# Performance work log

Hardware: AMD Instinct MI355X
Metric: run time of the kernel (lower is better)

The kernel has to match this reference:

```python
import jax, jax.numpy as jnp
import numpy as np
from jax import lax

K = 16  # knn_k


def _mlp(x, W1, b1, W2, b2):
    h = jax.nn.gelu(x @ W1 + b1, approximate=False)  # torch nn.GELU default = exact
    return h @ W2 + b2


def setup_inputs() -> dict:
    key = jax.random.key(0)
    ks = jax.random.split(key, 10)
    B, N, F, H = 8, 4096, 64, 128

    def xav(k, shape):
        fan_in = shape[0]
        return (jax.random.normal(k, shape, jnp.float32) / np.sqrt(fan_in)).astype(jnp.float32)

    return {
        "coords": jax.random.normal(ks[0], (B, N, 3), jnp.float32),
        "features": jax.random.normal(ks[1], (B, N, F), jnp.float32),
        "inv_W1": xav(ks[2], (6, H)), "inv_b1": jnp.zeros((H,), jnp.float32),
        "inv_W2": xav(ks[3], (H, H)), "inv_b2": jnp.zeros((H,), jnp.float32),
        "feat_W1": xav(ks[4], (F, H)), "feat_b1": jnp.zeros((H,), jnp.float32),
        "feat_W2": xav(ks[5], (H, H)), "feat_b2": jnp.zeros((H,), jnp.float32),
        "sh_W1": xav(ks[6], (2 * H, H)), "sh_b1": jnp.zeros((H,), jnp.float32),
        "sh_W2": xav(ks[7], (H, H)), "sh_b2": jnp.zeros((H,), jnp.float32),
        "g0_W": xav(ks[8], (H, 1)), "g0_b": jnp.zeros((1,), jnp.float32),
    }


def _local_geometry(coords):
    # coords: [B,N,3]
    B, N, _ = coords.shape
    k = min(K, N - 1)
    # squared pairwise distances (monotone in euclidean dist -> same kNN indices)
    sq = jnp.sum(coords * coords, axis=-1)                    # [B,N]
    dist2 = sq[:, :, None] + sq[:, None, :] - 2.0 * jnp.einsum("bnd,bmd->bnm", coords, coords)
    dist2 = lax.stop_gradient(dist2)
    eye = jnp.eye(N, dtype=bool)
    dist2 = jnp.where(eye[None], jnp.inf, dist2)
    _, idx = lax.top_k(-dist2, k)                             # smallest-k -> [B,N,k]
    neighbors = jax.vmap(lambda c, i: c[i])(coords, idx)      # [B,N,k,3]
    relative = neighbors - coords[:, :, None, :]              # [B,N,k,3]
    cov = jnp.einsum("bnki,bnkj->bnij", relative, relative) / float(k)  # [B,N,3,3]
    evals, evecs = jnp.linalg.eigh(cov)                       # ascending
    normals = evecs[..., 0]                                   # smallest-eigval eigenvector, [B,N,3]
    center = coords.mean(axis=1, keepdims=True)
    outward = coords - center
    orient = jnp.sign(jnp.sum(normals * outward, axis=-1, keepdims=True))
    orient = jnp.where(orient == 0, 1.0, orient)
    normals = normals * orient
    normals = normals / jnp.maximum(jnp.linalg.norm(normals, axis=-1, keepdims=True), 1e-6)
    radius = jnp.linalg.norm(relative, axis=-1).mean(axis=-1, keepdims=True)   # [B,N,1]
    centered_radius = jnp.linalg.norm(outward, axis=-1, keepdims=True)
    eig_sum = jnp.maximum(evals.sum(axis=-1, keepdims=True), 1e-6)
    dominance = evals[..., 2:3] / eig_sum
    invariants = jnp.concatenate([evals, radius, centered_radius, dominance], axis=-1)  # [B,N,6]
    return normals, invariants


def reference(coords, features, inv_W1, inv_b1, inv_W2, inv_b2,
              feat_W1, feat_b1, feat_W2, feat_b2,
              sh_W1, sh_b1, sh_W2, sh_b2, g0_W, g0_b):
    normals, invariants = _local_geometry(coords)
    inv_h = _mlp(invariants, inv_W1, inv_b1, inv_W2, inv_b2)
    feat_h = _mlp(features, feat_W1, feat_b1, feat_W2, feat_b2)
    hidden = _mlp(jnp.concatenate([inv_h, feat_h], axis=-1), sh_W1, sh_b1, sh_W2, sh_b2)
    scalar = hidden @ g0_W + g0_b                                   # grade 0, [B,N,1]
    plane = jnp.stack([normals[..., 0], normals[..., 1], -normals[..., 2],
                       -jnp.sum(coords * normals, axis=-1)], axis=-1)  # grade 1, [B,N,4]
    biv = jnp.concatenate([normals, jnp.zeros_like(normals)], axis=-1)  # grade 2, [B,N,6]
    point = jnp.concatenate([coords, jnp.ones(coords.shape[:-1] + (1,), coords.dtype)], axis=-1)  # grade 3 OPNS point
    zero4 = jnp.zeros(coords.shape[:-1] + (1,), coords.dtype)            # grade 4
    return jnp.concatenate([scalar, plane, biv, point, zero4], axis=-1)  # [B,N,16]
```

## Files before the change

### kernel.cpp

```cpp
#include <hip/hip_runtime.h>
#include <hip/hip_bf16.h>

#define BB 8
#define NN 4096
#define FF 64
#define HH 128
#define KNN 16

typedef __attribute__((ext_vector_type(8))) short bf16x8;
typedef __attribute__((ext_vector_type(4))) short bf16x4;
typedef __attribute__((ext_vector_type(4))) float f32x4;

#define OFF_iW2 0
#define OFF_fW1 16384
#define OFF_fW2 24576
#define OFF_sW1 40960
#define OFF_sW2 73728
#define HI_SZ   90112

__device__ __forceinline__ float sq3(float x, float y, float z) {
    return fmaf(z, z, fmaf(y, y, __fmul_rn(x, x)));
}
__device__ __forceinline__ float dist2f(float px, float py, float pz, float psq, float4 cc) {
    float t = fmaf(pz, cc.z, fmaf(py, cc.y, __fmul_rn(px, cc.x)));
    return __fsub_rn(__fadd_rn(psq, cc.w), __fmul_rn(2.0f, t));
}

__device__ __forceinline__ short f2bf(float x) {
    unsigned u = __float_as_uint(x);
    u += 0x7fffu + ((u >> 16) & 1u);
    return (short)(u >> 16);
}
__device__ __forceinline__ float bf2f(short s) {
    return __uint_as_float(((unsigned)(unsigned short)s) << 16);
}

extern "C" __global__ __launch_bounds__(256)
void k_prep(const float* __restrict__ coords, float4* __restrict__ coords4, float* __restrict__ center,
            const float* __restrict__ iW2, const float* __restrict__ fW1,
            const float* __restrict__ fW2, const float* __restrict__ sW1,
            const float* __restrict__ sW2, short* __restrict__ wbf) {
    const int bx = blockIdx.x, tid = threadIdx.x;
    __shared__ float rx[256], ry[256], rz[256];
    if (bx < 8) {
        const int b = bx;
        float sx = 0.f, sy = 0.f, sz = 0.f;
        for (int n = tid; n < NN; n += 256) {
            const float* c = coords + (size_t)(b * NN + n) * 3;
            float x = c[0], y = c[1], z = c[2];
            coords4[b * NN + n] = make_float4(x, y, z, sq3(x, y, z));
            sx += x; sy += y; sz += z;
        }
        rx[tid] = sx; ry[tid] = sy; rz[tid] = sz;
        __syncthreads();
        for (int s = 128; s > 0; s >>= 1) {
            if (tid < s) { rx[tid] += rx[tid + s]; ry[tid] += ry[tid + s]; rz[tid] += rz[tid + s]; }
            __syncthreads();
        }
        if (tid == 0) {
            center[b * 4 + 0] = rx[0] * (1.0f / NN);
            center[b * 4 + 1] = ry[0] * (1.0f / NN);
            center[b * 4 + 2] = rz[0] * (1.0f / NN);
        }
    } else {
        const int wb = bx - 8;
        const int w = wb >> 4;
        const int xb = wb & 15;
        const float* W; int K; int off;
        if (w == 0)      { W = iW2; K = 128; off = OFF_iW2; }
        else if (w == 1) { W = fW1; K = 64;  off = OFF_fW1; }
        else if (w == 2) { W = fW2; K = 128; off = OFF_fW2; }
        else if (w == 3) { W = sW1; K = 256; off = OFF_sW1; }
        else             { W = sW2; K = 128; off = OFF_sW2; }
        short* hi = wbf + off;
        short* lo = wbf + HI_SZ + off;
        const int total = K * 128;
        for (int e = xb * 256 + tid; e < total; e += 4096) {
            int j = e & 7, lane = (e >> 3) & 63, ct = (e >> 9) & 7, kb = e >> 12;
            int k = kb * 32 + (lane >> 4) * 8 + j;
            int n = ct * 16 + (lane & 15);
            float v = W[k * 128 + n];
            short h = f2bf(v);
            float r = v - bf2f(h);
            hi[e] = h; lo[e] = f2bf(r);
        }
    }
}

#define JROT(app, aqq, apq, arp, arq, vp0, vp1, vp2, vq0, vq1, vq2) { \
    float tau_ = (aqq - app) / (2.0f * apq); \
    float tt_ = copysignf(1.0f, tau_) / (fabsf(tau_) + sqrtf(1.0f + tau_ * tau_)); \
    if (apq == 0.0f) tt_ = 0.0f; \
    float cc_ = 1.0f / sqrtf(1.0f + tt_ * tt_); \
    float ss_ = tt_ * cc_; \
    float app_n = cc_*cc_*app - 2.0f*cc_*ss_*apq + ss_*ss_*aqq; \
    float aqq_n = ss_*ss_*app + 2.0f*cc_*ss_*apq + cc_*cc_*aqq; \
    float apq_n = cc_*ss_*(app - aqq) + (cc_*cc_ - ss_*ss_)*apq; \
    float arp_n = cc_*arp - ss_*arq; \
    float arq_n = ss_*arp + cc_*arq; \
    app = app_n; aqq = aqq_n; apq = apq_n; arp = arp_n; arq = arq_n; \
    float t0_ = cc_*vp0 - ss_*vq0, t1_ = cc_*vp1 - ss_*vq1, t2_ = cc_*vp2 - ss_*vq2; \
    vq0 = ss_*vp0 + cc_*vq0; vq1 = ss_*vp1 + cc_*vq1; vq2 = ss_*vp2 + cc_*vq2; \
    vp0 = t0_; vp1 = t1_; vp2 = t2_; }

#define SWAPF(a, b) { float sw_ = a; a = b; b = sw_; }

__device__ __forceinline__ void ce(float& a, float& b) {
    float mn = fminf(a, b);
    b = fmaxf(a, b);
    a = mn;
}

__device__ __forceinline__ void sort16(float (&d)[16]) {
    ce(d[0],d[1]); ce(d[2],d[3]); ce(d[0],d[2]); ce(d[1],d[3]); ce(d[1],d[2]);
    ce(d[4],d[5]); ce(d[6],d[7]); ce(d[4],d[6]); ce(d[5],d[7]); ce(d[5],d[6]);
    ce(d[0],d[4]); ce(d[2],d[6]); ce(d[2],d[4]);
    ce(d[1],d[5]); ce(d[3],d[7]); ce(d[3],d[5]);
    ce(d[1],d[2]); ce(d[3],d[4]); ce(d[5],d[6]);
    ce(d[8],d[9]); ce(d[10],d[11]); ce(d[8],d[10]); ce(d[9],d[11]); ce(d[9],d[10]);
    ce(d[12],d[13]); ce(d[14],d[15]); ce(d[12],d[14]); ce(d[13],d[15]); ce(d[13],d[14]);
    ce(d[8],d[12]); ce(d[10],d[14]); ce(d[10],d[12]);
    ce(d[9],d[13]); ce(d[11],d[15]); ce(d[11],d[13]);
    ce(d[9],d[10]); ce(d[11],d[12]); ce(d[13],d[14]);
    ce(d[0],d[8]); ce(d[4],d[12]); ce(d[4],d[8]);
    ce(d[2],d[10]); ce(d[6],d[14]); ce(d[6],d[10]);
    ce(d[2],d[4]); ce(d[6],d[8]); ce(d[10],d[12]);
    ce(d[1],d[9]); ce(d[5],d[13]); ce(d[5],d[9]);
    ce(d[3],d[11]); ce(d[7],d[15]); ce(d[7],d[11]);
    ce(d[3],d[5]); ce(d[7],d[9]); ce(d[11],d[13]);
    ce(d[1],d[2]); ce(d[3],d[4]); ce(d[5],d[6]); ce(d[7],d[8]);
    ce(d[9],d[10]); ce(d[11],d[12]); ce(d[13],d[14]);
}

__device__ __forceinline__ void merge16(float (&dk)[16], float (&d)[16]) {
#pragma unroll
    for (int i = 0; i < 8; i++) {
        float a  = fminf(dk[i], d[15 - i]);
        float b2 = fminf(dk[15 - i], d[i]);
        d[i] = a; d[15 - i] = b2;
    }
#pragma unroll
    for (int j = 8; j > 0; j >>= 1)
#pragma unroll
        for (int i = 0; i < 16; i++) {
            int l = i ^ j;
            if (l > i) ce(d[i], d[l]);
        }
#pragma unroll
    for (int i = 0; i < 16; i++) dk[i] = d[i];
}

__device__ __forceinline__ void sort16i(int (&d)[16]) {
#pragma unroll
    for (int k = 2; k <= 16; k <<= 1) {
#pragma unroll
        for (int j = k >> 1; j > 0; j >>= 1) {
#pragma unroll
            for (int i = 0; i < 16; i++) {
                int l = i ^ j;
                if (l > i) {
                    int a = d[i], bq = d[l];
                    int mn = a < bq ? a : bq;
                    int mx = a < bq ? bq : a;
                    if ((i & k) == 0) { d[i] = mn; d[l] = mx; }
                    else              { d[i] = mx; d[l] = mn; }
                }
            }
        }
    }
}

extern "C" __global__ __launch_bounds__(512, 8)
void k_knn(const float4* __restrict__ coords4, const float* __restrict__ center,
           float* __restrict__ inv8g, float* __restrict__ out) {
    const int blk = blockIdx.x;
    const int b = blk >> 7;
    const int chunk = blk & 127;
    const int tid = threadIdx.x;
    const int h = tid & 15;
    const int pid = tid >> 4;
    const int n = chunk * 32 + pid;
    const float4* __restrict__ C = coords4 + b * NN;

    __shared__ __align__(16) float4 tile[1024];
    __shared__ unsigned short slist[512];
    __shared__ unsigned short tlist[256];
    __shared__ int cnt_s[32];
    __shared__ int cnt_t[32];

    if (tid < 32) { cnt_s[tid] = 0; cnt_t[tid] = 0; }

    float4 me = C[n];
    const float px = me.x, py = me.y, pz = me.z, psq = me.w;
    const float INF = __builtin_inff();

    float dk[KNN];
#pragma unroll
    for (int i = 0; i < KNN; i++) dk[i] = INF;

    for (int r = 0; r < 4; r++) {
        __syncthreads();
        tile[tid] = C[r * 1024 + tid];
        tile[tid + 512] = C[r * 1024 + tid + 512];
        __syncthreads();
#pragma unroll
        for (int bt = 0; bt < 4; bt++) {
            float d[16];
#pragma unroll
            for (int i = 0; i < 16; i++) {
                float4 cc = tile[bt * 256 + i * 16 + h];
                float dd = dist2f(px, py, pz, psq, cc);
                int g = r * 1024 + bt * 256 + i * 16 + h;
                d[i] = (g == n) ? INF : dd;
            }
            sort16(d);
            merge16(dk, d);
        }
    }

#pragma unroll
    for (int m = 1; m <= 8; m <<= 1) {
        float o[16];
#pragma unroll
        for (int i = 0; i < KNN; i++) o[i] = __shfl_xor(dk[i], m);
        merge16(dk, o);
    }
    const float d15 = dk[15];

    for (int r = 0; r < 4; r++) {
        __syncthreads();
        tile[tid] = C[r * 1024 + tid];
        tile[tid + 512] = C[r * 1024 + tid + 512];
        __syncthreads();
#pragma unroll 4
        for (int j16 = 0; j16 < 64; j16++) {
            float4 cc = tile[j16 * 16 + h];
            float d = dist2f(px, py, pz, psq, cc);
            int g = r * 1024 + j16 * 16 + h;
            if (g != n && d <= d15) {
                if (d < d15) {
                    int pos = atomicAdd(&cnt_s[pid], 1);
                    if (pos < 16) slist[pid * 16 + pos] = (unsigned short)g;
                } else {
                    int pos = atomicAdd(&cnt_t[pid], 1);
                    if (pos < 8) tlist[pid * 8 + pos] = (unsigned short)g;
                }
            }
        }
    }
    __syncthreads();

    if (tid < 32) {
        const int np = chunk * 32 + tid;
        float4 pme = C[np];
        int ns = cnt_s[tid]; ns = ns > 15 ? 15 : ns;
        int ids[16];
#pragma unroll
        for (int j = 0; j < 16; j++) {
            int tj = j - ns; tj = tj < 0 ? 0 : (tj > 7 ? 7 : tj);
            int sid = (int)slist[tid * 16 + j];
            int tie = (int)tlist[tid * 8 + tj];
            ids[j] = (j < ns) ? sid : tie;
        }
        sort16i(ids);

        float cxx = 0.f, cxy = 0.f, cxz = 0.f, cyy = 0.f, cyz = 0.f, czz = 0.f, radsum = 0.f;
#pragma unroll
        for (int j = 0; j < KNN; j++) {
            float4 cc = C[ids[j]];
            float rx = __fsub_rn(cc.x, pme.x), ry = __fsub_rn(cc.y, pme.y), rz = __fsub_rn(cc.z, pme.z);
            cxx = __fadd_rn(cxx, __fmul_rn(rx, rx));
            cxy = __fadd_rn(cxy, __fmul_rn(rx, ry));
            cxz = __fadd_rn(cxz, __fmul_rn(rx, rz));
            cyy = __fadd_rn(cyy, __fmul_rn(ry, ry));
            cyz = __fadd_rn(cyz, __fmul_rn(ry, rz));
            czz = __fadd_rn(czz, __fmul_rn(rz, rz));
            float rr = __fadd_rn(__fadd_rn(__fmul_rn(rx, rx), __fmul_rn(ry, ry)), __fmul_rn(rz, rz));
            radsum = __fadd_rn(radsum, sqrtf(rr));
        }
        const float inv_k = 1.0f / KNN;
        float a00 = cxx * inv_k, a01 = cxy * inv_k, a02 = cxz * inv_k;
        float a11 = cyy * inv_k, a12 = cyz * inv_k, a22 = czz * inv_k;

        float V00 = 1.f, V01 = 0.f, V02 = 0.f;
        float V10 = 0.f, V11 = 1.f, V12 = 0.f;
        float V20 = 0.f, V21 = 0.f, V22 = 1.f;
        for (int sweep = 0; sweep < 6; sweep++) {
            JROT(a00, a11, a01, a02, a12, V00, V10, V20, V01, V11, V21);
            JROT(a00, a22, a02, a01, a12, V00, V10, V20, V02, V12, V22);
            JROT(a11, a22, a12, a01, a02, V01, V11, V21, V02, V12, V22);
        }
        float e0 = a00, e1 = a11, e2 = a22;
        float x0 = V00, y0 = V10, z0 = V20;
        float x1 = V01, y1 = V11, z1 = V21;
        float x2 = V02, y2 = V12, z2 = V22;
        if (e0 > e1) { SWAPF(e0, e1); SWAPF(x0, x1); SWAPF(y0, y1); SWAPF(z0, z1); }
        if (e1 > e2) { SWAPF(e1, e2); SWAPF(x1, x2); SWAPF(y1, y2); SWAPF(z1, z2); }
        if (e0 > e1) { SWAPF(e0, e1); SWAPF(x0, x1); SWAPF(y0, y1); SWAPF(z0, z1); }

        float cx = center[b * 4 + 0], cy = center[b * 4 + 1], cz = center[b * 4 + 2];
        float ox = __fsub_rn(pme.x, cx), oy = __fsub_rn(pme.y, cy), oz = __fsub_rn(pme.z, cz);
        float dt = __fadd_rn(__fadd_rn(__fmul_rn(x0, ox), __fmul_rn(y0, oy)), __fmul_rn(z0, oz));
        float sgn = (dt >= 0.0f) ? 1.0f : -1.0f;
        x0 *= sgn; y0 *= sgn; z0 *= sgn;
        float nrm = sqrtf(__fadd_rn(__fadd_rn(__fmul_rn(x0, x0), __fmul_rn(y0, y0)), __fmul_rn(z0, z0)));
        float den = fmaxf(nrm, 1e-6f);
        x0 = x0 / den; y0 = y0 / den; z0 = z0 / den;

        float radius = radsum * inv_k;
        float crad = sqrtf(__fadd_rn(__fadd_rn(__fmul_rn(ox, ox), __fmul_rn(oy, oy)), __fmul_rn(oz, oz)));
        float esum = fmaxf(__fadd_rn(__fadd_rn(e0, e1), e2), 1e-6f);
        float dom = e2 / esum;

        float* ip = inv8g + (size_t)(b * NN + np) * 8;
        ip[0] = e0; ip[1] = e1; ip[2] = e2; ip[3] = radius; ip[4] = crad; ip[5] = dom;
        ip[6] = 0.f; ip[7] = 0.f;

        float pd = __fadd_rn(__fadd_rn(__fmul_rn(pme.x, x0), __fmul_rn(pme.y, y0)), __fmul_rn(pme.z, z0));
        float4* o = (float4*)(out + (size_t)(b * NN + np) * 16);
        o[0] = make_float4(0.0f, x0, y0, -z0);
        o[1] = make_float4(-pd, x0, y0, z0);
        o[2] = make_float4(0.0f, 0.0f, 0.0f, pme.x);
        o[3] = make_float4(pme.y, pme.z, 1.0f, 0.0f);
    }
}

__device__ __forceinline__ float gelu_exact(float x) {
    return 0.5f * x * (1.0f + erff(x * 0.70710678118654752440f));
}

template <int KB, bool INIT>
__device__ __forceinline__ void gemm_mfma(const short* Ab, const short* __restrict__ whi,
                                          const short* __restrict__ wlo,
                                          const float* __restrict__ bias,
                                          int wid, int lane, f32x4 acc[2]) {
    const int m16 = lane & 15, quad = lane >> 4;
    if (INIT) {
        float b0 = bias[wid * 16 + m16];
        acc[0] = (f32x4){b0, b0, b0, b0};
        acc[1] = acc[0];
    }
#pragma unroll 1
    for (int kb = 0; kb < KB; kb++) {
        bf16x8 a0 = *(const bf16x8*)(Ab + m16 * 136 + kb * 32 + quad * 8);
        bf16x8 a1 = *(const bf16x8*)(Ab + (m16 + 16) * 136 + kb * 32 + quad * 8);
        const int off = ((kb * 8 + wid) * 64 + lane) * 8;
        bf16x8 bh = *(const bf16x8*)(whi + off);
        bf16x8 bl = *(const bf16x8*)(wlo + off);
        acc[0] = __builtin_amdgcn_mfma_f32_16x16x32_bf16(a0, bh, acc[0], 0, 0, 0);
        acc[0] = __builtin_amdgcn_mfma_f32_16x16x32_bf16(a0, bl, acc[0], 0, 0, 0);
        acc[1] = __builtin_amdgcn_mfma_f32_16x16x32_bf16(a1, bh, acc[1], 0, 0, 0);
        acc[1] = __builtin_amdgcn_mfma_f32_16x16x32_bf16(a1, bl, acc[1], 0, 0, 0);
    }
}

__device__ __forceinline__ void acc_to_bf(short* dst, f32x4 acc[2], int wid, int lane, bool dogelu) {
    const int m16 = lane & 15, quad = lane >> 4;
#pragma unroll
    for (int mt = 0; mt < 2; mt++)
#pragma unroll
        for (int i = 0; i < 4; i++) {
            float v = acc[mt][i];
            if (dogelu) v = gelu_exact(v);
            dst[(mt * 16 + quad * 4 + i) * 136 + wid * 16 + m16] = f2bf(v);
        }
}

extern "C" __global__ __launch_bounds__(512, 8)
void k_mlp(const float* __restrict__ features, const short* __restrict__ wbf,
           const float* __restrict__ iW1, const float* __restrict__ ib1,
           const float* __restrict__ ib2,
           const float* __restrict__ fb1, const float* __restrict__ fb2,
           const float* __restrict__ sb1, const float* __restrict__ sb2,
           const float* __restrict__ gW, const float* __restrict__ gb,
           const float* __restrict__ inv8g, float* __restrict__ out) {
    const int blk = blockIdx.x;
    const int b = blk >> 7;
    const int chunk = blk & 127;
    const int tid = threadIdx.x;

    __shared__ __align__(16) float inv8[256];
    __shared__ float sc[32];
    __shared__ __align__(16) short Abf[32 * 136];
    __shared__ __align__(16) short FHbf[32 * 136];

    const int wid = tid >> 6, lane = tid & 63;
    const short* w_iW2h = wbf + OFF_iW2; const short* w_iW2l = wbf + HI_SZ + OFF_iW2;
    const short* w_fW1h = wbf + OFF_fW1; const short* w_fW1l = wbf + HI_SZ + OFF_fW1;
    const short* w_fW2h = wbf + OFF_fW2; const short* w_fW2l = wbf + HI_SZ + OFF_fW2;
    const short* w_sW1h = wbf + OFF_sW1; const short* w_sW1l = wbf + HI_SZ + OFF_sW1;
    const short* w_sW2h = wbf + OFF_sW2; const short* w_sW2l = wbf + HI_SZ + OFF_sW2;
    f32x4 acc[2];

    if (tid < 256) inv8[tid] = inv8g[(size_t)(b * NN + chunk * 32) * 8 + tid];
    if (tid < 32) sc[tid] = gb[0];
    {
        int row = tid >> 4, c4 = (tid & 15) * 4;
        const float* s = features + (size_t)(b * NN + chunk * 32 + row) * FF + c4;
        float4 v = *(const float4*)s;
        bf16x4 pk;
        pk[0] = f2bf(v.x); pk[1] = f2bf(v.y); pk[2] = f2bf(v.z); pk[3] = f2bf(v.w);
        *(bf16x4*)(Abf + row * 136 + c4) = pk;
    }
    __syncthreads();

    gemm_mfma<2, true>(Abf, w_fW1h, w_fW1l, fb1, wid, lane, acc);
    __syncthreads();
    acc_to_bf(Abf, acc, wid, lane, true);
    __syncthreads();

    gemm_mfma<4, true>(Abf, w_fW2h, w_fW2l, fb2, wid, lane, acc);
    __syncthreads();
    acc_to_bf(FHbf, acc, wid, lane, false);

    {
        const int cg = tid & 31, pg = tid >> 5;
        const int c0 = cg * 4, p0 = pg * 2;
        float4 bb = *(const float4*)(ib1 + c0);
        float a2[2][4];
#pragma unroll
        for (int i = 0; i < 2; i++) { a2[i][0] = bb.x; a2[i][1] = bb.y; a2[i][2] = bb.z; a2[i][3] = bb.w; }
#pragma unroll
        for (int k = 0; k < 6; k++) {
            float4 w = *(const float4*)(iW1 + k * HH + c0);
#pragma unroll
            for (int i = 0; i < 2; i++) {
                float a = inv8[(p0 + i) * 8 + k];
                a2[i][0] = fmaf(a, w.x, a2[i][0]);
                a2[i][1] = fmaf(a, w.y, a2[i][1]);
                a2[i][2] = fmaf(a, w.z, a2[i][2]);
                a2[i][3] = fmaf(a, w.w, a2[i][3]);
            }
        }
#pragma unroll
        for (int i = 0; i < 2; i++) {
            bf16x4 pk;
            pk[0] = f2bf(gelu_exact(a2[i][0])); pk[1] = f2bf(gelu_exact(a2[i][1]));
            pk[2] = f2bf(gelu_exact(a2[i][2])); pk[3] = f2bf(gelu_exact(a2[i][3]));
            *(bf16x4*)(Abf + (p0 + i) * 136 + c0) = pk;
        }
    }
    __syncthreads();

    gemm_mfma<4, true>(Abf, w_iW2h, w_iW2l, ib2, wid, lane, acc);
    __syncthreads();
    acc_to_bf(Abf, acc, wid, lane, false);
    __syncthreads();

    gemm_mfma<4, true>(Abf, w_sW1h, w_sW1l, sb1, wid, lane, acc);
    gemm_mfma<4, false>(FHbf, w_sW1h + 16384, w_sW1l + 16384, nullptr, wid, lane, acc);
    __syncthreads();
    acc_to_bf(Abf, acc, wid, lane, true);
    __syncthreads();

    gemm_mfma<4, true>(Abf, w_sW2h, w_sW2l, sb2, wid, lane, acc);
    {
        const int m16 = lane & 15, quad = lane >> 4;
        float g = gW[wid * 16 + m16];
#pragma unroll
        for (int mt = 0; mt < 2; mt++)
#pragma unroll
            for (int i = 0; i < 4; i++)
                atomicAdd(&sc[mt * 16 + quad * 4 + i], acc[mt][i] * g);
    }
    __syncthreads();
    if (tid < 32) out[(size_t)(b * NN + chunk * 32 + tid) * 16] = sc[tid];
}

extern "C" void kernel_launch(void* const* d_in, const int* in_sizes, int n_in,
                              void* d_out, int out_size, void* d_ws, size_t ws_size,
                              hipStream_t stream) {
    const float* coords   = (const float*)d_in[0];
    const float* features = (const float*)d_in[1];
    const float* iW1 = (const float*)d_in[2],  * ib1 = (const float*)d_in[3];
    const float* iW2 = (const float*)d_in[4],  * ib2 = (const float*)d_in[5];
    const float* fW1 = (const float*)d_in[6],  * fb1 = (const float*)d_in[7];
    const float* fW2 = (const float*)d_in[8],  * fb2 = (const float*)d_in[9];
    const float* sW1 = (const float*)d_in[10], * sb1 = (const float*)d_in[11];
    const float* sW2 = (const float*)d_in[12], * sb2 = (const float*)d_in[13];
    const float* gW  = (const float*)d_in[14], * gb  = (const float*)d_in[15];
    float* out = (float*)d_out;

    char* ws = (char*)d_ws;
    float4* coords4 = (float4*)ws;
    float* center   = (float*)(ws + 524288);
    short* wbf      = (short*)(ws + 524416);
    float* inv8g    = (float*)(ws + 884864);

    hipLaunchKernelGGL(k_prep, dim3(88), dim3(256), 0, stream,
                       coords, coords4, center, iW2, fW1, fW2, sW1, sW2, wbf);
    hipLaunchKernelGGL(k_knn, dim3(1024), dim3(512), 0, stream, coords4, center, inv8g, out);
    hipLaunchKernelGGL(k_mlp, dim3(1024), dim3(512), 0, stream, features, wbf,
                       iW1, ib1, ib2, fb1, fb2, sb1, sb2, gW, gb, inv8g, out);
}
```

Measured before the change: 263.8 us.

## Double-buffer kNN tiles, hoist self-exclusion, and process 64 points per MLP block

The kNN kernel now double-buffers the coordinate tile in shared memory, so the next 1024-point tile loads while the current one is scanned, removing one barrier per round. The self-exclusion compare now runs only in the tile that holds the query point. merge16 now works in place instead of copying back. The MLP kernel handles two 32-point sub-tiles per block, reusing each loaded weight fragment for twice the MFMA work, and launches half as many blocks with a lower occupancy hint. This doubles LDS use and may raise register pressure.

```diff
diff --git a/kernel.cpp b/kernel.cpp
--- a/kernel.cpp
+++ b/kernel.cpp
@@ -132,22 +132,20 @@
     ce(d[9],d[10]); ce(d[11],d[12]); ce(d[13],d[14]);
 }
 
-__device__ __forceinline__ void merge16(float (&dk)[16], float (&d)[16]) {
+__device__ __forceinline__ void merge16(float (&dk)[16], const float (&d)[16]) {
 #pragma unroll
     for (int i = 0; i < 8; i++) {
         float a  = fminf(dk[i], d[15 - i]);
         float b2 = fminf(dk[15 - i], d[i]);
-        d[i] = a; d[15 - i] = b2;
+        dk[i] = a; dk[15 - i] = b2;
     }
 #pragma unroll
     for (int j = 8; j > 0; j >>= 1)
 #pragma unroll
         for (int i = 0; i < 16; i++) {
             int l = i ^ j;
-            if (l > i) ce(d[i], d[l]);
-        }
-#pragma unroll
-    for (int i = 0; i < 16; i++) dk[i] = d[i];
+            if (l > i) ce(dk[i], dk[l]);
+        }
 }
 
 __device__ __forceinline__ void sort16i(int (&d)[16]) {
@@ -168,6 +166,23 @@
             }
         }
     }
+}
+
+template <bool CHK>
+__device__ __forceinline__ void batch16(const float4* __restrict__ T, int bt, int h, int sl_local,
+                                        float px, float py, float pz, float psq,
+                                        float (&dk)[16]) {
+    const float INF = __builtin_inff();
+    float d[16];
+#pragma unroll
+    for (int i = 0; i < 16; i++) {
+        float4 cc = T[bt * 256 + i * 16 + h];
+        float dd = dist2f(px, py, pz, psq, cc);
+        if (CHK) d[i] = (bt * 256 + i * 16 + h) == sl_local ? INF : dd;
+        else     d[i] = dd;
+    }
+    sort16(d);
+    merge16(dk, d);
 }
 
 extern "C" __global__ __launch_bounds__(512, 8)
@@ -182,7 +197,7 @@
     const int n = chunk * 32 + pid;
     const float4* __restrict__ C = coords4 + b * NN;
 
-    __shared__ __align__(16) float4 tile[1024];
+    __shared__ __align__(16) float4 tile[2][1024];
     __shared__ unsigned short slist[512];
     __shared__ unsigned short tlist[256];
     __shared__ int cnt_s[32];
@@ -194,29 +209,40 @@
     const float px = me.x, py = me.y, pz = me.z, psq = me.w;
     const float INF = __builtin_inff();
 
+    const int r_self  = chunk >> 5;
+    const int bt_self = (chunk >> 3) & 3;
+    const int sl_local = n & 1023;
+
     float dk[KNN];
 #pragma unroll
     for (int i = 0; i < KNN; i++) dk[i] = INF;
 
+    tile[0][tid] = C[tid];
+    tile[0][tid + 512] = C[tid + 512];
     for (int r = 0; r < 4; r++) {
         __syncthreads();
-        tile[tid] = C[r * 1024 + tid];
-        tile[tid + 512] = C[r * 1024 + tid + 512];
-        __syncthreads();
-#pragma unroll
-        for (int bt = 0; bt < 4; bt++) {
-            float d[16];
-#pragma unroll
-            for (int i = 0; i < 16; i++) {
-                float4 cc = tile[bt * 256 + i * 16 + h];
-                float dd = dist2f(px, py, pz, psq, cc);
-                int g = r * 1024 + bt * 256 + i * 16 + h;
-                d[i] = (g == n) ? INF : dd;
-            }
-            sort16(d);
-            merge16(dk, d);
-        }
-    }
+        if (r < 3) {
+            tile[(r + 1) & 1][tid] = C[(r + 1) * 1024 + tid];
+            tile[(r + 1) & 1][tid + 512] = C[(r + 1) * 1024 + tid + 512];
+        }
+        const float4* T = tile[r & 1];
+        if (r != r_self) {
+            batch16<false>(T, 0, h, sl_local, px, py, pz, psq, dk);
+            batch16<false>(T, 1, h, sl_local, px, py, pz, psq, dk);
+            batch16<false>(T, 2, h, sl_local, px, py, pz, psq, dk);
+            batch16<false>(T, 3, h, sl_local, px, py, pz, psq, dk);
+        } else {
+#pragma unroll
+            for (int bt = 0; bt < 4; bt++) {
+                if (bt == bt_self) batch16<true>(T, bt, h, sl_local, px, py, pz, psq, dk);
+                else               batch16<false>(T, bt, h, sl_local, px, py, pz, psq, dk);
+            }
+        }
+    }
+
+    __syncthreads();
+    tile[0][tid] = C[tid];
+    tile[0][tid + 512] = C[tid + 512];
 
 #pragma unroll
     for (int m = 1; m <= 8; m <<= 1) {
@@ -229,21 +255,42 @@
 
     for (int r = 0; r < 4; r++) {
         __syncthreads();
-        tile[tid] = C[r * 1024 + tid];
-        tile[tid + 512] = C[r * 1024 + tid + 512];
-        __syncthreads();
+        if (r < 3) {
+            tile[(r + 1) & 1][tid] = C[(r + 1) * 1024 + tid];
+            tile[(r + 1) & 1][tid + 512] = C[(r + 1) * 1024 + tid + 512];
+        }
+        const float4* T = tile[r & 1];
+        if (r != r_self) {
 #pragma unroll 4
-        for (int j16 = 0; j16 < 64; j16++) {
-            float4 cc = tile[j16 * 16 + h];
-            float d = dist2f(px, py, pz, psq, cc);
-            int g = r * 1024 + j16 * 16 + h;
-            if (g != n && d <= d15) {
-                if (d < d15) {
-                    int pos = atomicAdd(&cnt_s[pid], 1);
-                    if (pos < 16) slist[pid * 16 + pos] = (unsigned short)g;
-                } else {
-                    int pos = atomicAdd(&cnt_t[pid], 1);
-                    if (pos < 8) tlist[pid * 8 + pos] = (unsigned short)g;
+            for (int j16 = 0; j16 < 64; j16++) {
+                float4 cc = T[j16 * 16 + h];
+                float d = dist2f(px, py, pz, psq, cc);
+                if (d <= d15) {
+                    int g = r * 1024 + j16 * 16 + h;
+                    if (d < d15) {
+                        int pos = atomicAdd(&cnt_s[pid], 1);
+                        if (pos < 16) slist[pid * 16 + pos] = (unsigned short)g;
+                    } else {
+                        int pos = atomicAdd(&cnt_t[pid], 1);
+                        if (pos < 8) tlist[pid * 8 + pos] = (unsigned short)g;
+                    }
+                }
+            }
+        } else {
+#pragma unroll 4
+            for (int j16 = 0; j16 < 64; j16++) {
+                float4 cc = T[j16 * 16 + h];
+                float d = dist2f(px, py, pz, psq, cc);
+                int cl = j16 * 16 + h;
+                if (cl != sl_local && d <= d15) {
+                    int g = r * 1024 + cl;
+                    if (d < d15) {
+                        int pos = atomicAdd(&cnt_s[pid], 1);
+                        if (pos < 16) slist[pid * 16 + pos] = (unsigned short)g;
+                    } else {
+                        int pos = atomicAdd(&cnt_t[pid], 1);
+                        if (pos < 8) tlist[pid * 8 + pos] = (unsigned short)g;
+                    }
                 }
             }
         }
@@ -330,27 +377,35 @@
 }
 
 template <int KB, bool INIT>
-__device__ __forceinline__ void gemm_mfma(const short* Ab, const short* __restrict__ whi,
-                                          const short* __restrict__ wlo,
-                                          const float* __restrict__ bias,
-                                          int wid, int lane, f32x4 acc[2]) {
+__device__ __forceinline__ void gemm_mfma2(const short* Ab0, const short* Ab1,
+                                           const short* __restrict__ whi,
+                                           const short* __restrict__ wlo,
+                                           const float* __restrict__ bias,
+                                           int wid, int lane, f32x4 acc0[2], f32x4 acc1[2]) {
     const int m16 = lane & 15, quad = lane >> 4;
     if (INIT) {
         float b0 = bias[wid * 16 + m16];
-        acc[0] = (f32x4){b0, b0, b0, b0};
-        acc[1] = acc[0];
+        acc0[0] = (f32x4){b0, b0, b0, b0};
+        acc0[1] = acc0[0]; acc1[0] = acc0[0]; acc1[1] = acc0[0];
     }
 #pragma unroll 1
     for (int kb = 0; kb < KB; kb++) {
-        bf16x8 a0 = *(const bf16x8*)(Ab + m16 * 136 + kb * 32 + quad * 8);
-        bf16x8 a1 = *(const bf16x8*)(Ab + (m16 + 16) * 136 + kb * 32 + quad * 8);
         const int off = ((kb * 8 + wid) * 64 + lane) * 8;
         bf16x8 bh = *(const bf16x8*)(whi + off);
         bf16x8 bl = *(const bf16x8*)(wlo + off);
-        acc[0] = __builtin_amdgcn_mfma_f32_16x16x32_bf16(a0, bh, acc[0], 0, 0, 0);
-        acc[0] = __builtin_amdgcn_mfma_f32_16x16x32_bf16(a0, bl, acc[0], 0, 0, 0);
-        acc[1] = __builtin_amdgcn_mfma_f32_16x16x32_bf16(a1, bh, acc[1], 0, 0, 0);
-        acc[1] = __builtin_amdgcn_mfma_f32_16x16x32_bf16(a1, bl, acc[1], 0, 0, 0);
+        const int ao = m16 * 136 + kb * 32 + quad * 8;
+        bf16x8 a00 = *(const bf16x8*)(Ab0 + ao);
+        bf16x8 a01 = *(const bf16x8*)(Ab0 + ao + 16 * 136);
+        bf16x8 a10 = *(const bf16x8*)(Ab1 + ao);
+        bf16x8 a11 = *(const bf16x8*)(Ab1 + ao + 16 * 136);
+        acc0[0] = __builtin_amdgcn_mfma_f32_16x16x32_bf16(a00, bh, acc0[0], 0, 0, 0);
+        acc0[0] = __builtin_amdgcn_mfma_f32_16x16x32_bf16(a00, bl, acc0[0], 0, 0, 0);
+        acc0[1] = __builtin_amdgcn_mfma_f32_16x16x32_bf16(a01, bh, acc0[1], 0, 0, 0);
+        acc0[1] = __builtin_amdgcn_mfma_f32_16x16x32_bf16(a01, bl, acc0[1], 0, 0, 0);
+        acc1[0] = __builtin_amdgcn_mfma_f32_16x16x32_bf16(a10, bh, acc1[0], 0, 0, 0);
+        acc1[0] = __builtin_amdgcn_mfma_f32_16x16x32_bf16(a10, bl, acc1[0], 0, 0, 0);
+        acc1[1] = __builtin_amdgcn_mfma_f32_16x16x32_bf16(a11, bh, acc1[1], 0, 0, 0);
+        acc1[1] = __builtin_amdgcn_mfma_f32_16x16x32_bf16(a11, bl, acc1[1], 0, 0, 0);
     }
 }
 
@@ -366,7 +421,7 @@
         }
 }
 
-extern "C" __global__ __launch_bounds__(512, 8)
+extern "C" __global__ __launch_bounds__(512, 4)
 void k_mlp(const float* __restrict__ features, const short* __restrict__ wbf,
            const float* __restrict__ iW1, const float* __restrict__ ib1,
            const float* __restrict__ ib2,
@@ -375,14 +430,15 @@
            const float* __restrict__ gW, const float* __restrict__ gb,
            const float* __restrict__ inv8g, float* __restrict__ out) {
     const int blk = blockIdx.x;
-    const int b = blk >> 7;
-    const int chunk = blk & 127;
+    const int b = blk >> 6;
+    const int cg = blk & 63;
+    const int p0g = cg * 64;
     const int tid = threadIdx.x;
 
-    __shared__ __align__(16) float inv8[256];
-    __shared__ float sc[32];
-    __shared__ __align__(16) short Abf[32 * 136];
-    __shared__ __align__(16) short FHbf[32 * 136];
+    __shared__ __align__(16) float inv8[2][256];
+    __shared__ float sc[2][32];
+    __shared__ __align__(16) short Abf[2][32 * 136];
+    __shared__ __align__(16) short FHbf[2][32 * 136];
 
     const int wid = tid >> 6, lane = tid & 63;
     const short* w_iW2h = wbf + OFF_iW2; const short* w_iW2l = wbf + HI_SZ + OFF_iW2;
@@ -390,81 +446,91 @@
     const short* w_fW2h = wbf + OFF_fW2; const short* w_fW2l = wbf + HI_SZ + OFF_fW2;
     const short* w_sW1h = wbf + OFF_sW1; const short* w_sW1l = wbf + HI_SZ + OFF_sW1;
     const short* w_sW2h = wbf + OFF_sW2; const short* w_sW2l = wbf + HI_SZ + OFF_sW2;
-    f32x4 acc[2];
-
-    if (tid < 256) inv8[tid] = inv8g[(size_t)(b * NN + chunk * 32) * 8 + tid];
-    if (tid < 32) sc[tid] = gb[0];
+    f32x4 acc0[2], acc1[2];
+
+    inv8[tid >> 8][tid & 255] = inv8g[(size_t)(b * NN + p0g) * 8 + tid];
+    if (tid < 64) sc[tid >> 5][tid & 31] = gb[0];
     {
-        int row = tid >> 4, c4 = (tid & 15) * 4;
-        const float* s = features + (size_t)(b * NN + chunk * 32 + row) * FF + c4;
-        float4 v = *(const float4*)s;
-        bf16x4 pk;
-        pk[0] = f2bf(v.x); pk[1] = f2bf(v.y); pk[2] = f2bf(v.z); pk[3] = f2bf(v.w);
-        *(bf16x4*)(Abf + row * 136 + c4) = pk;
-    }
-    __syncthreads();
-
-    gemm_mfma<2, true>(Abf, w_fW1h, w_fW1l, fb1, wid, lane, acc);
-    __syncthreads();
-    acc_to_bf(Abf, acc, wid, lane, true);
-    __syncthreads();
-
-    gemm_mfma<4, true>(Abf, w_fW2h, w_fW2l, fb2, wid, lane, acc);
-    __syncthreads();
-    acc_to_bf(FHbf, acc, wid, lane, false);
+        int row = tid >> 3, c8 = (tid & 7) * 8;
+        const float* s = features + (size_t)(b * NN + p0g + row) * FF + c8;
+        float4 v0 = *(const float4*)s, v1 = *(const float4*)(s + 4);
+        bf16x8 pk;
+        pk[0] = f2bf(v0.x); pk[1] = f2bf(v0.y); pk[2] = f2bf(v0.z); pk[3] = f2bf(v0.w);
+        pk[4] = f2bf(v1.x); pk[5] = f2bf(v1.y); pk[6] = f2bf(v1.z); pk[7] = f2bf(v1.w);
+        *(bf16x8*)(Abf[row >> 5] + (row & 31) * 136 + c8) = pk;
+    }
+    __syncthreads();
+
+    gemm_mfma2<2, true>(Abf[0], Abf[1], w_fW1h, w_fW1l, fb1, wid, lane, acc0, acc1);
+    __syncthreads();
+    acc_to_bf(Abf[0], acc0, wid, lane, true);
+    acc_to_bf(Abf[1], acc1, wid, lane, true);
+    __syncthreads();
+
+    gemm_mfma2<4, true>(Abf[0], Abf[1], w_fW2h, w_fW2l, fb2, wid, lane, acc0, acc1);
+    __syncthreads();
+    acc_to_bf(FHbf[0], acc0, wid, lane, false);
+    acc_to_bf(FHbf[1], acc1, wid, lane, false);
 
     {
-        const int cg = tid & 31, pg = tid >> 5;
-        const int c0 = cg * 4, p0 = pg * 2;
+        const int cgr = tid & 31, pg = tid >> 5;
+        const int c0 = cgr * 4, p0 = pg * 2;
         float4 bb = *(const float4*)(ib1 + c0);
-        float a2[2][4];
-#pragma unroll
-        for (int i = 0; i < 2; i++) { a2[i][0] = bb.x; a2[i][1] = bb.y; a2[i][2] = bb.z; a2[i][3] = bb.w; }
-#pragma unroll
-        for (int k = 0; k < 6; k++) {
-            float4 w = *(const float4*)(iW1 + k * HH + c0);
+#pragma unroll
+        for (int c = 0; c < 2; c++) {
+            float a2[2][4];
+#pragma unroll
+            for (int i = 0; i < 2; i++) { a2[i][0] = bb.x; a2[i][1] = bb.y; a2[i][2] = bb.z; a2[i][3] = bb.w; }
+#pragma unroll
+            for (int k = 0; k < 6; k++) {
+                float4 w = *(const float4*)(iW1 + k * HH + c0);
+#pragma unroll
+                for (int i = 0; i < 2; i++) {
+                    float a = inv8[c][(p0 + i) * 8 + k];
+                    a2[i][0] = fmaf(a, w.x, a2[i][0]);
+                    a2[i][1] = fmaf(a, w.y, a2[i][1]);
+                    a2[i][2] = fmaf(a, w.z, a2[i][2]);
+                    a2[i][3] = fmaf(a, w.w, a2[i][3]);
+                }
+            }
 #pragma unroll
             for (int i = 0; i < 2; i++) {
-                float a = inv8[(p0 + i) * 8 + k];
-                a2[i][0] = fmaf(a, w.x, a2[i][0]);
-                a2[i][1] = fmaf(a, w.y, a2[i][1]);
-                a2[i][2] = fmaf(a, w.z, a2[i][2]);
-                a2[i][3] = fmaf(a, w.w, a2[i][3]);
-            }
-        }
-#pragma unroll
-        for (int i = 0; i < 2; i++) {
-            bf16x4 pk;
-            pk[0] = f2bf(gelu_exact(a2[i][0])); pk[1] = f2bf(gelu_exact(a2[i][1]));
-            pk[2] = f2bf(gelu_exact(a2[i][2])); pk[3] = f2bf(gelu_exact(a2[i][3]));
-            *(bf16x4*)(Abf + (p0 + i) * 136 + c0) = pk;
-        }
-    }
-    __syncthreads();
-
-    gemm_mfma<4, true>(Abf, w_iW2h, w_iW2l, ib2, wid, lane, acc);
-    __syncthreads();
-    acc_to_bf(Abf, acc, wid, lane, false);
-    __syncthreads();
-
-    gemm_mfma<4, true>(Abf, w_sW1h, w_sW1l, sb1, wid, lane, acc);
-    gemm_mfma<4, false>(FHbf, w_sW1h + 16384, w_sW1l + 16384, nullptr, wid, lane, acc);
-    __syncthreads();
-    acc_to_bf(Abf, acc, wid, lane, true);
-    __syncthreads();
-
-    gemm_mfma<4, true>(Abf, w_sW2h, w_sW2l, sb2, wid, lane, acc);
+                bf16x4 pk;
+                pk[0] = f2bf(gelu_exact(a2[i][0])); pk[1] = f2bf(gelu_exact(a2[i][1]));
+                pk[2] = f2bf(gelu_exact(a2[i][2])); pk[3] = f2bf(gelu_exact(a2[i][3]));
+                *(bf16x4*)(Abf[c] + (p0 + i) * 136 + c0) = pk;
+            }
+        }
+    }
+    __syncthreads();
+
+    gemm_mfma2<4, true>(Abf[0], Abf[1], w_iW2h, w_iW2l, ib2, wid, lane, acc0, acc1);
+    __syncthreads();
+    acc_to_bf(Abf[0], acc0, wid, lane, false);
+    acc_to_bf(Abf[1], acc1, wid, lane, false);
+    __syncthreads();
+
+    gemm_mfma2<4, true>(Abf[0], Abf[1], w_sW1h, w_sW1l, sb1, wid, lane, acc0, acc1);
+    gemm_mfma2<4, false>(FHbf[0], FHbf[1], w_sW1h + 16384, w_sW1l + 16384, nullptr, wid, lane, acc0, acc1);
+    __syncthreads();
+    acc_to_bf(Abf[0], acc0, wid, lane, true);
+    acc_to_bf(Abf[1], acc1, wid, lane, true);
+    __syncthreads();
+
+    gemm_mfma2<4, true>(Abf[0], Abf[1], w_sW2h, w_sW2l, sb2, wid, lane, acc0, acc1);
     {
         const int m16 = lane & 15, quad = lane >> 4;
         float g = gW[wid * 16 + m16];
 #pragma unroll
         for (int mt = 0; mt < 2; mt++)
 #pragma unroll
-            for (int i = 0; i < 4; i++)
-                atomicAdd(&sc[mt * 16 + quad * 4 + i], acc[mt][i] * g);
-    }
-    __syncthreads();
-    if (tid < 32) out[(size_t)(b * NN + chunk * 32 + tid) * 16] = sc[tid];
+            for (int i = 0; i < 4; i++) {
+                atomicAdd(&sc[0][mt * 16 + quad * 4 + i], acc0[mt][i] * g);
+                atomicAdd(&sc[1][mt * 16 + quad * 4 + i], acc1[mt][i] * g);
+            }
+    }
+    __syncthreads();
+    if (tid < 64) out[(size_t)(b * NN + p0g + tid) * 16] = sc[tid >> 5][tid & 31];
 }
 
 extern "C" void kernel_launch(void* const* d_in, const int* in_sizes, int n_in,
@@ -490,6 +556,6 @@
     hipLaunchKernelGGL(k_prep, dim3(88), dim3(256), 0, stream,
                        coords, coords4, center, iW2, fW1, fW2, sW1, sW2, wbf);
     hipLaunchKernelGGL(k_knn, dim3(1024), dim3(512), 0, stream, coords4, center, inv8g, out);
-    hipLaunchKernelGGL(k_mlp, dim3(1024), dim3(512), 0, stream, features, wbf,
+    hipLaunchKernelGGL(k_mlp, dim3(512), dim3(512), 0, stream, features, wbf,
                        iW1, ib1, ib2, fb1, fb2, sb1, sb2, gW, gb, inv8g, out);
 }
```

Result: slower. 285.0 us (+8.0%).
